# Kernel optimization log

Measured on AMD Instinct MI355X. Metric: run time of the kernel, lower is better.

Reference implementation:

```python
import jax, jax.numpy as jnp
import numpy as np

N_NODES = 50000
N_EDGES = 600000
D = 128
NUM_LAYERS = 2
ALPHA = 0.5
EPS = 1e-12  # torch F.normalize eps


def setup_inputs() -> dict:
    key = jax.random.key(0)
    k1, k2, k3, k4, k5 = jax.random.split(key, 5)
    x = jax.random.normal(k1, (N_NODES, D), dtype=jnp.float32)
    edge_attr = jax.random.normal(k2, (N_EDGES, D), dtype=jnp.float32)
    question_emb = jax.random.normal(k3, (D,), dtype=jnp.float32)
    src = jax.random.randint(k4, (N_EDGES,), 0, N_NODES)
    dst = jax.random.randint(k5, (N_EDGES,), 0, N_NODES)
    edge_index = jnp.stack([src, dst], axis=0).astype(jnp.int64)
    return {"x": x, "edge_attr": edge_attr, "question_emb": question_emb, "edge_index": edge_index}


def reference(x, edge_attr, question_emb, edge_index):
    num_nodes = x.shape[0]
    # edge similarity: cosine of edge_attr rows vs question vector
    ea = edge_attr / jnp.maximum(jnp.linalg.norm(edge_attr, axis=1, keepdims=True), EPS)
    q = question_emb / jnp.maximum(jnp.linalg.norm(question_emb), EPS)
    edge_sim = ea @ q  # [E]
    src, dst = edge_index[0], edge_index[1]
    # degree of destination nodes (constant across layers)
    deg = jax.ops.segment_sum(jnp.ones_like(edge_sim), dst, num_segments=num_nodes)
    deg = jnp.clip(deg, 1.0)[:, None]  # [N,1]
    for _ in range(NUM_LAYERS):
        msgs = x[src] * edge_sim[:, None]                              # [E,D] gather + scale
        x_new = jax.ops.segment_sum(msgs, dst, num_segments=num_nodes)  # [N,D] scatter-add
        x_new = x_new / deg                                             # mean aggregation
        x = ALPHA * x + (1.0 - ALPHA) * x_new                           # residual blend
    return x
```

## Files before the change

### kernel.cpp

```cpp
#include <hip/hip_runtime.h>
#include <hip/hip_fp16.h>
#include <math.h>

#define N_NODES 50000
#define N_EDGES 600000
#define D 128
#define EPS 1e-12f
#define CAP 64

__global__ void cvt_kernel(const float* __restrict__ x, ushort* __restrict__ xh) {
    int i = blockIdx.x * blockDim.x + threadIdx.x;
    if (i >= N_NODES * D / 4) return;
    float4 v = ((const float4*)x)[i];
    ushort4 h;
    h.x = __half_as_ushort(__float2half(v.x));
    h.y = __half_as_ushort(__float2half(v.y));
    h.z = __half_as_ushort(__float2half(v.z));
    h.w = __half_as_ushort(__float2half(v.w));
    ((ushort4*)xh)[i] = h;
}

__global__ void edge_fill_kernel(const float* __restrict__ ea,
                                 const float* __restrict__ q,
                                 const int* __restrict__ src,
                                 const int* __restrict__ dst,
                                 int* __restrict__ cnt,
                                 int2* __restrict__ bucket,
                                 int* __restrict__ ovf_cnt,
                                 int4* __restrict__ ovf) {
    int gid  = blockIdx.x * blockDim.x + threadIdx.x;
    int wave = gid >> 6;
    if (wave >= N_EDGES / 2) return;
    int lane = threadIdx.x & 63;
    int half = lane >> 5;
    int l32  = lane & 31;
    int e    = 2 * wave + half;

    float4 v  = ((const float4*)(ea + (size_t)e * D))[l32];
    float4 qv = ((const float4*)q)[l32];
    float dot = v.x * qv.x + v.y * qv.y + v.z * qv.z + v.w * qv.w;
    float ss  = v.x * v.x + v.y * v.y + v.z * v.z + v.w * v.w;
    float qs  = qv.x * qv.x + qv.y * qv.y + qv.z * qv.z + qv.w * qv.w;
    #pragma unroll
    for (int off = 16; off > 0; off >>= 1) {
        dot += __shfl_xor(dot, off);
        ss  += __shfl_xor(ss, off);
        qs  += __shfl_xor(qs, off);
    }
    if (l32 == 0) {
        float sim = dot / (fmaxf(sqrtf(ss), EPS) * fmaxf(sqrtf(qs), EPS));
        int d    = dst[e];
        int slot = atomicAdd(&cnt[d], 1);
        if (slot < CAP) {
            bucket[(size_t)d * CAP + slot] = make_int2(src[e], __float_as_int(sim));
        } else {
            int oi = atomicAdd(ovf_cnt, 1);
            ovf[oi] = make_int4(d, src[e], __float_as_int(sim), 0);
        }
    }
}

__global__ void agg_kernel(const ushort* __restrict__ xh,
                           const float* __restrict__ xin,
                           const int* __restrict__ cnt,
                           const int2* __restrict__ bucket,
                           float* __restrict__ xout,
                           ushort* __restrict__ xh_out) {
    int gid  = blockIdx.x * blockDim.x + threadIdx.x;
    int node = gid >> 6;
    if (node >= N_NODES) return;
    int lane = threadIdx.x & 63;
    int half = lane >> 5;
    int l32  = lane & 31;

    int n  = cnt[node];
    int nb = (n < CAP) ? n : CAP;

    int sl = 0; float wl = 0.0f;
    if (lane < nb) {
        int2 p = bucket[(size_t)node * CAP + lane];
        sl = p.x; wl = __int_as_float(p.y);
    }

    float4 acc = make_float4(0.0f, 0.0f, 0.0f, 0.0f);
    #pragma unroll 2
    for (int j = half; j < nb; j += 2) {
        int   s = __shfl(sl, j);
        float w = __shfl(wl, j);
        ushort4 hv = ((const ushort4*)(xh + (size_t)s * D))[l32];
        acc.x += __half2float(__ushort_as_half(hv.x)) * w;
        acc.y += __half2float(__ushort_as_half(hv.y)) * w;
        acc.z += __half2float(__ushort_as_half(hv.z)) * w;
        acc.w += __half2float(__ushort_as_half(hv.w)) * w;
    }
    acc.x += __shfl_xor(acc.x, 32);
    acc.y += __shfl_xor(acc.y, 32);
    acc.z += __shfl_xor(acc.z, 32);
    acc.w += __shfl_xor(acc.w, 32);

    if (half == 0) {
        float di = 1.0f / fmaxf((float)n, 1.0f);
        float4 a = ((const float4*)(xin + (size_t)node * D))[l32];
        float4 o;
        o.x = 0.5f * a.x + 0.5f * acc.x * di;
        o.y = 0.5f * a.y + 0.5f * acc.y * di;
        o.z = 0.5f * a.z + 0.5f * acc.z * di;
        o.w = 0.5f * a.w + 0.5f * acc.w * di;
        ((float4*)(xout + (size_t)node * D))[l32] = o;
        if (xh_out) {
            ushort4 h;
            h.x = __half_as_ushort(__float2half(o.x));
            h.y = __half_as_ushort(__float2half(o.y));
            h.z = __half_as_ushort(__float2half(o.z));
            h.w = __half_as_ushort(__float2half(o.w));
            ((ushort4*)(xh_out + (size_t)node * D))[l32] = h;
        }
    }
}

__global__ void ovf_fix_kernel(const float* __restrict__ xin,
                               const int* __restrict__ cnt,
                               const int* __restrict__ ovf_cnt,
                               const int4* __restrict__ ovf,
                               float* __restrict__ xout,
                               ushort* __restrict__ xh_out) {
    int t = threadIdx.x;
    int m = *ovf_cnt;
    for (int i = 0; i < m; ++i) {
        int4 p = ovf[i];
        int d = p.x, s = p.y;
        float w  = __int_as_float(p.z);
        float di = 1.0f / fmaxf((float)cnt[d], 1.0f);
        float r  = xout[(size_t)d * D + t] + 0.5f * w * di * xin[(size_t)s * D + t];
        xout[(size_t)d * D + t] = r;
        if (xh_out) xh_out[(size_t)d * D + t] = __half_as_ushort(__float2half(r));
    }
}

extern "C" void kernel_launch(void* const* d_in, const int* in_sizes, int n_in,
                              void* d_out, int out_size, void* d_ws, size_t ws_size,
                              hipStream_t stream) {
    const float* x  = (const float*)d_in[0];
    const float* ea = (const float*)d_in[1];
    const float* q  = (const float*)d_in[2];
    const int*   ei = (const int*)d_in[3];
    const int* src = ei;
    const int* dst = ei + N_EDGES;
    float* out = (float*)d_out;

    float*  x1      = (float*)d_ws;
    ushort* xh      = (ushort*)(x1 + (size_t)N_NODES * D);
    ushort* x1h     = xh + (size_t)N_NODES * D;
    int2*   bucket  = (int2*)(x1h + (size_t)N_NODES * D);
    int*    cnt     = (int*)(bucket + (size_t)N_NODES * CAP);
    int*    ovf_cnt = cnt + N_NODES;
    int4*   ovf     = (int4*)(cnt + N_NODES + 4);

    hipMemsetAsync(cnt, 0, (size_t)(N_NODES + 4) * sizeof(int), stream);

    cvt_kernel<<<(N_NODES * D / 4 + 255) / 256, 256, 0, stream>>>(x, xh);

    {
        long long threads = (long long)(N_EDGES / 2) * 64;
        int blocks = (int)((threads + 255) / 256);
        edge_fill_kernel<<<blocks, 256, 0, stream>>>(ea, q, src, dst,
                                                     cnt, bucket, ovf_cnt, ovf);
    }

    const int agg_blocks = (int)(((long long)N_NODES * 64 + 255) / 256);
    agg_kernel<<<agg_blocks, 256, 0, stream>>>(xh,  x,  cnt, bucket, x1,  x1h);
    ovf_fix_kernel<<<1, 128, 0, stream>>>(x,  cnt, ovf_cnt, ovf, x1, x1h);
    agg_kernel<<<agg_blocks, 256, 0, stream>>>(x1h, x1, cnt, bucket, out, (ushort*)0);
    ovf_fix_kernel<<<1, 128, 0, stream>>>(x1, cnt, ovf_cnt, ovf, out, (ushort*)0);
}
```

Baseline: 536.6 us.

## Batch 16 independent neighbor row loads per wave in aggregation kernel

The aggregation kernel now has each full 64-lane wave read one half2 (4 bytes) of every neighbor row, instead of splitting the wave into two halves that alternate neighbors and read 8 bytes each. Neighbor offsets are computed up front and 16 gathers are issued back to back before any accumulation, which raises memory-level parallelism and drops the final cross-half reduction. Lanes with no edge default to the node's own row with zero weight, so the first 16 loads are always issued even for low-degree nodes. That adds wasted loads and more registers per thread, which may reduce occupancy.

```diff
diff --git a/kernel.cpp b/kernel.cpp
--- a/kernel.cpp
+++ b/kernel.cpp
@@ -70,51 +70,73 @@
     int node = gid >> 6;
     if (node >= N_NODES) return;
     int lane = threadIdx.x & 63;
-    int half = lane >> 5;
-    int l32  = lane & 31;
 
     int n  = cnt[node];
     int nb = (n < CAP) ? n : CAP;
 
-    int sl = 0; float wl = 0.0f;
+    int sl = node; float wl = 0.0f;
     if (lane < nb) {
         int2 p = bucket[(size_t)node * CAP + lane];
         sl = p.x; wl = __int_as_float(p.y);
     }
 
-    float4 acc = make_float4(0.0f, 0.0f, 0.0f, 0.0f);
-    #pragma unroll 2
-    for (int j = half; j < nb; j += 2) {
+    const uint* base = (const uint*)xh;
+    float accx = 0.0f, accy = 0.0f;
+
+    uint off0[16];
+    #pragma unroll
+    for (int j = 0; j < 16; ++j) {
+        int s = __shfl(sl, j);
+        off0[j] = (uint)s * (D / 2) + lane;
+    }
+    uint u0[16];
+    #pragma unroll
+    for (int j = 0; j < 16; ++j) u0[j] = base[off0[j]];
+    #pragma unroll
+    for (int j = 0; j < 16; ++j) {
+        float w = __shfl(wl, j);
+        __half2 h2 = *reinterpret_cast<__half2*>(&u0[j]);
+        float2 f = __half22float2(h2);
+        accx += f.x * w; accy += f.y * w;
+    }
+
+    if (nb > 16) {
+        uint off1[16];
+        #pragma unroll
+        for (int j = 0; j < 16; ++j) {
+            int s = __shfl(sl, 16 + j);
+            off1[j] = (uint)s * (D / 2) + lane;
+        }
+        uint u1[16];
+        #pragma unroll
+        for (int j = 0; j < 16; ++j) u1[j] = base[off1[j]];
+        #pragma unroll
+        for (int j = 0; j < 16; ++j) {
+            float w = __shfl(wl, 16 + j);
+            __half2 h2 = *reinterpret_cast<__half2*>(&u1[j]);
+            float2 f = __half22float2(h2);
+            accx += f.x * w; accy += f.y * w;
+        }
+    }
+
+    for (int j = 32; j < nb; ++j) {
         int   s = __shfl(sl, j);
         float w = __shfl(wl, j);
-        ushort4 hv = ((const ushort4*)(xh + (size_t)s * D))[l32];
-        acc.x += __half2float(__ushort_as_half(hv.x)) * w;
-        acc.y += __half2float(__ushort_as_half(hv.y)) * w;
-        acc.z += __half2float(__ushort_as_half(hv.z)) * w;
-        acc.w += __half2float(__ushort_as_half(hv.w)) * w;
+        uint u = base[(uint)s * (D / 2) + lane];
+        __half2 h2 = *reinterpret_cast<__half2*>(&u);
+        float2 f = __half22float2(h2);
+        accx += f.x * w; accy += f.y * w;
     }
-    acc.x += __shfl_xor(acc.x, 32);
-    acc.y += __shfl_xor(acc.y, 32);
-    acc.z += __shfl_xor(acc.z, 32);
-    acc.w += __shfl_xor(acc.w, 32);
 
-    if (half == 0) {
-        float di = 1.0f / fmaxf((float)n, 1.0f);
-        float4 a = ((const float4*)(xin + (size_t)node * D))[l32];
-        float4 o;
-        o.x = 0.5f * a.x + 0.5f * acc.x * di;
-        o.y = 0.5f * a.y + 0.5f * acc.y * di;
-        o.z = 0.5f * a.z + 0.5f * acc.z * di;
-        o.w = 0.5f * a.w + 0.5f * acc.w * di;
-        ((float4*)(xout + (size_t)node * D))[l32] = o;
-        if (xh_out) {
-            ushort4 h;
-            h.x = __half_as_ushort(__float2half(o.x));
-            h.y = __half_as_ushort(__float2half(o.y));
-            h.z = __half_as_ushort(__float2half(o.z));
-            h.w = __half_as_ushort(__float2half(o.w));
-            ((ushort4*)(xh_out + (size_t)node * D))[l32] = h;
-        }
+    float di = 1.0f / fmaxf((float)n, 1.0f);
+    float2 a = ((const float2*)xin)[(size_t)node * (D / 2) + lane];
+    float2 o;
+    o.x = 0.5f * a.x + 0.5f * accx * di;
+    o.y = 0.5f * a.y + 0.5f * accy * di;
+    ((float2*)xout)[(size_t)node * (D / 2) + lane] = o;
+    if (xh_out) {
+        __half2 hh = __floats2half2_rn(o.x, o.y);
+        ((uint*)xh_out)[(size_t)node * (D / 2) + lane] = *reinterpret_cast<uint*>(&hh);
     }
 }
 
```

Measured after the change: 521.7 us. 1.03x faster.

## Restructure aggregation into 16-lane groups with batched gathers and fused overflow handling

Applied to the files above, without the earlier changes.

Aggregation now splits each wavefront into four 16-lane groups, each loading a full 256-byte half-precision row with 16-byte loads. Neighbour gathers are issued in batches of four to raise memory-level parallelism, and padding lanes reuse a valid source with zero weight. The separate overflow-fix kernels and the memset are folded into the aggregation and conversion kernels, which removes launches. Edge-attribute reads use nontemporal loads to avoid polluting the cache. Every aggregation thread now scans the overflow list, which costs extra reads if overflow ever occurs.

```diff
diff --git a/kernel.cpp b/kernel.cpp
--- a/kernel.cpp
+++ b/kernel.cpp
@@ -8,16 +8,21 @@
 #define EPS 1e-12f
 #define CAP 64
 
-__global__ void cvt_kernel(const float* __restrict__ x, ushort* __restrict__ xh) {
+typedef float f32x4 __attribute__((ext_vector_type(4)));
+
+__global__ void prep_kernel(const float* __restrict__ x, ushort* __restrict__ xh,
+                            int* __restrict__ cnt) {
     int i = blockIdx.x * blockDim.x + threadIdx.x;
-    if (i >= N_NODES * D / 4) return;
-    float4 v = ((const float4*)x)[i];
-    ushort4 h;
-    h.x = __half_as_ushort(__float2half(v.x));
-    h.y = __half_as_ushort(__float2half(v.y));
-    h.z = __half_as_ushort(__float2half(v.z));
-    h.w = __half_as_ushort(__float2half(v.w));
-    ((ushort4*)xh)[i] = h;
+    if (i < N_NODES + 4) cnt[i] = 0;
+    if (i < N_NODES * D / 4) {
+        float4 v = ((const float4*)x)[i];
+        ushort4 h;
+        h.x = __half_as_ushort(__float2half(v.x));
+        h.y = __half_as_ushort(__float2half(v.y));
+        h.z = __half_as_ushort(__float2half(v.z));
+        h.w = __half_as_ushort(__float2half(v.w));
+        ((ushort4*)xh)[i] = h;
+    }
 }
 
 __global__ void edge_fill_kernel(const float* __restrict__ ea,
@@ -36,7 +41,7 @@
     int l32  = lane & 31;
     int e    = 2 * wave + half;
 
-    float4 v  = ((const float4*)(ea + (size_t)e * D))[l32];
+    f32x4 v  = __builtin_nontemporal_load(((const f32x4*)(ea + (size_t)e * D)) + l32);
     float4 qv = ((const float4*)q)[l32];
     float dot = v.x * qv.x + v.y * qv.y + v.z * qv.z + v.w * qv.w;
     float ss  = v.x * v.x + v.y * v.y + v.z * v.z + v.w * v.w;
@@ -60,80 +65,121 @@
     }
 }
 
+__device__ __forceinline__ void acc8(uint4 v, float w,
+                                     float& a0, float& a1, float& a2, float& a3,
+                                     float& a4, float& a5, float& a6, float& a7) {
+    float2 f;
+    f = __half22float2(*reinterpret_cast<const __half2*>(&v.x)); a0 += f.x * w; a1 += f.y * w;
+    f = __half22float2(*reinterpret_cast<const __half2*>(&v.y)); a2 += f.x * w; a3 += f.y * w;
+    f = __half22float2(*reinterpret_cast<const __half2*>(&v.z)); a4 += f.x * w; a5 += f.y * w;
+    f = __half22float2(*reinterpret_cast<const __half2*>(&v.w)); a6 += f.x * w; a7 += f.y * w;
+}
+
 __global__ void agg_kernel(const ushort* __restrict__ xh,
                            const float* __restrict__ xin,
                            const int* __restrict__ cnt,
                            const int2* __restrict__ bucket,
+                           const int* __restrict__ ovf_cnt,
+                           const int4* __restrict__ ovf,
                            float* __restrict__ xout,
                            ushort* __restrict__ xh_out) {
     int gid  = blockIdx.x * blockDim.x + threadIdx.x;
     int node = gid >> 6;
     if (node >= N_NODES) return;
     int lane = threadIdx.x & 63;
-    int half = lane >> 5;
-    int l32  = lane & 31;
+    int g    = lane >> 4;
+    int l16  = lane & 15;
 
     int n  = cnt[node];
     int nb = (n < CAP) ? n : CAP;
 
-    int sl = 0; float wl = 0.0f;
+    int sl = node; float wl = 0.0f;
     if (lane < nb) {
         int2 p = bucket[(size_t)node * CAP + lane];
         sl = p.x; wl = __int_as_float(p.y);
     }
-
-    float4 acc = make_float4(0.0f, 0.0f, 0.0f, 0.0f);
-    #pragma unroll 2
-    for (int j = half; j < nb; j += 2) {
-        int   s = __shfl(sl, j);
-        float w = __shfl(wl, j);
-        ushort4 hv = ((const ushort4*)(xh + (size_t)s * D))[l32];
-        acc.x += __half2float(__ushort_as_half(hv.x)) * w;
-        acc.y += __half2float(__ushort_as_half(hv.y)) * w;
-        acc.z += __half2float(__ushort_as_half(hv.z)) * w;
-        acc.w += __half2float(__ushort_as_half(hv.w)) * w;
-    }
-    acc.x += __shfl_xor(acc.x, 32);
-    acc.y += __shfl_xor(acc.y, 32);
-    acc.z += __shfl_xor(acc.z, 32);
-    acc.w += __shfl_xor(acc.w, 32);
-
-    if (half == 0) {
+    int s0 = __shfl(sl, 0);
+    if (lane >= nb) sl = s0;
+
+    const uint4* base = (const uint4*)xh;
+    float a0 = 0, a1 = 0, a2 = 0, a3 = 0, a4 = 0, a5 = 0, a6 = 0, a7 = 0;
+
+    {
+        int   e0 = g,      e1 = 4 + g,  e2 = 8 + g,  e3 = 12 + g;
+        int   s_0 = __shfl(sl, e0), s_1 = __shfl(sl, e1), s_2 = __shfl(sl, e2), s_3 = __shfl(sl, e3);
+        float w_0 = __shfl(wl, e0), w_1 = __shfl(wl, e1), w_2 = __shfl(wl, e2), w_3 = __shfl(wl, e3);
+        uint4 v_0 = base[(size_t)s_0 * 16 + l16];
+        uint4 v_1 = base[(size_t)s_1 * 16 + l16];
+        uint4 v_2 = base[(size_t)s_2 * 16 + l16];
+        uint4 v_3 = base[(size_t)s_3 * 16 + l16];
+        acc8(v_0, w_0, a0, a1, a2, a3, a4, a5, a6, a7);
+        acc8(v_1, w_1, a0, a1, a2, a3, a4, a5, a6, a7);
+        acc8(v_2, w_2, a0, a1, a2, a3, a4, a5, a6, a7);
+        acc8(v_3, w_3, a0, a1, a2, a3, a4, a5, a6, a7);
+    }
+    if (nb > 16) {
+        int   e0 = 16 + g, e1 = 20 + g, e2 = 24 + g, e3 = 28 + g;
+        int   s_0 = __shfl(sl, e0), s_1 = __shfl(sl, e1), s_2 = __shfl(sl, e2), s_3 = __shfl(sl, e3);
+        float w_0 = __shfl(wl, e0), w_1 = __shfl(wl, e1), w_2 = __shfl(wl, e2), w_3 = __shfl(wl, e3);
+        uint4 v_0 = base[(size_t)s_0 * 16 + l16];
+        uint4 v_1 = base[(size_t)s_1 * 16 + l16];
+        uint4 v_2 = base[(size_t)s_2 * 16 + l16];
+        uint4 v_3 = base[(size_t)s_3 * 16 + l16];
+        acc8(v_0, w_0, a0, a1, a2, a3, a4, a5, a6, a7);
+        acc8(v_1, w_1, a0, a1, a2, a3, a4, a5, a6, a7);
+        acc8(v_2, w_2, a0, a1, a2, a3, a4, a5, a6, a7);
+        acc8(v_3, w_3, a0, a1, a2, a3, a4, a5, a6, a7);
+    }
+    for (int js = 8; 4 * js < nb; ++js) {
+        int   e0 = 4 * js + g;
+        int   s_0 = __shfl(sl, e0);
+        float w_0 = __shfl(wl, e0);
+        uint4 v_0 = base[(size_t)s_0 * 16 + l16];
+        acc8(v_0, w_0, a0, a1, a2, a3, a4, a5, a6, a7);
+    }
+
+    #define RED(A) A += __shfl_xor(A, 16); A += __shfl_xor(A, 32);
+    RED(a0) RED(a1) RED(a2) RED(a3) RED(a4) RED(a5) RED(a6) RED(a7)
+    #undef RED
+
+    int m = *ovf_cnt;
+    if (m > 0) {
+        for (int i = 0; i < m; ++i) {
+            int4 p = ovf[i];
+            if (p.x == node) {
+                float w = __int_as_float(p.z);
+                const float* r = xin + (size_t)p.y * D + l16 * 8;
+                a0 += w * r[0]; a1 += w * r[1]; a2 += w * r[2]; a3 += w * r[3];
+                a4 += w * r[4]; a5 += w * r[5]; a6 += w * r[6]; a7 += w * r[7];
+            }
+        }
+    }
+
+    if (g < 2) {
         float di = 1.0f / fmaxf((float)n, 1.0f);
-        float4 a = ((const float4*)(xin + (size_t)node * D))[l32];
+        size_t idx = (size_t)node * 32 + l16 * 2 + g;
+        float4 a = ((const float4*)xin)[idx];
         float4 o;
-        o.x = 0.5f * a.x + 0.5f * acc.x * di;
-        o.y = 0.5f * a.y + 0.5f * acc.y * di;
-        o.z = 0.5f * a.z + 0.5f * acc.z * di;
-        o.w = 0.5f * a.w + 0.5f * acc.w * di;
-        ((float4*)(xout + (size_t)node * D))[l32] = o;
+        if (g == 0) {
+            o.x = 0.5f * a.x + 0.5f * a0 * di;
+            o.y = 0.5f * a.y + 0.5f * a1 * di;
+            o.z = 0.5f * a.z + 0.5f * a2 * di;
+            o.w = 0.5f * a.w + 0.5f * a3 * di;
+        } else {
+            o.x = 0.5f * a.x + 0.5f * a4 * di;
+            o.y = 0.5f * a.y + 0.5f * a5 * di;
+            o.z = 0.5f * a.z + 0.5f * a6 * di;
+            o.w = 0.5f * a.w + 0.5f * a7 * di;
+        }
+        ((float4*)xout)[idx] = o;
         if (xh_out) {
-            ushort4 h;
-            h.x = __half_as_ushort(__float2half(o.x));
-            h.y = __half_as_ushort(__float2half(o.y));
-            h.z = __half_as_ushort(__float2half(o.z));
-            h.w = __half_as_ushort(__float2half(o.w));
-            ((ushort4*)(xh_out + (size_t)node * D))[l32] = h;
-        }
-    }
-}
-
-__global__ void ovf_fix_kernel(const float* __restrict__ xin,
-                               const int* __restrict__ cnt,
-                               const int* __restrict__ ovf_cnt,
-                               const int4* __restrict__ ovf,
-                               float* __restrict__ xout,
-                               ushort* __restrict__ xh_out) {
-    int t = threadIdx.x;
-    int m = *ovf_cnt;
-    for (int i = 0; i < m; ++i) {
-        int4 p = ovf[i];
-        int d = p.x, s = p.y;
-        float w  = __int_as_float(p.z);
-        float di = 1.0f / fmaxf((float)cnt[d], 1.0f);
-        float r  = xout[(size_t)d * D + t] + 0.5f * w * di * xin[(size_t)s * D + t];
-        xout[(size_t)d * D + t] = r;
-        if (xh_out) xh_out[(size_t)d * D + t] = __half_as_ushort(__float2half(r));
+            __half2 h0 = __floats2half2_rn(o.x, o.y);
+            __half2 h1 = __floats2half2_rn(o.z, o.w);
+            uint2 u;
+            u.x = *reinterpret_cast<uint*>(&h0);
+            u.y = *reinterpret_cast<uint*>(&h1);
+            ((uint2*)xh_out)[idx] = u;
+        }
     }
 }
 
@@ -156,9 +202,7 @@
     int*    ovf_cnt = cnt + N_NODES;
     int4*   ovf     = (int4*)(cnt + N_NODES + 4);
 
-    hipMemsetAsync(cnt, 0, (size_t)(N_NODES + 4) * sizeof(int), stream);
-
-    cvt_kernel<<<(N_NODES * D / 4 + 255) / 256, 256, 0, stream>>>(x, xh);
+    prep_kernel<<<(N_NODES * D / 4 + 255) / 256, 256, 0, stream>>>(x, xh, cnt);
 
     {
         long long threads = (long long)(N_EDGES / 2) * 64;
@@ -168,8 +212,6 @@
     }
 
     const int agg_blocks = (int)(((long long)N_NODES * 64 + 255) / 256);
-    agg_kernel<<<agg_blocks, 256, 0, stream>>>(xh,  x,  cnt, bucket, x1,  x1h);
-    ovf_fix_kernel<<<1, 128, 0, stream>>>(x,  cnt, ovf_cnt, ovf, x1, x1h);
-    agg_kernel<<<agg_blocks, 256, 0, stream>>>(x1h, x1, cnt, bucket, out, (ushort*)0);
-    ovf_fix_kernel<<<1, 128, 0, stream>>>(x1, cnt, ovf_cnt, ovf, out, (ushort*)0);
-}
+    agg_kernel<<<agg_blocks, 256, 0, stream>>>(xh,  x,  cnt, bucket, ovf_cnt, ovf, x1,  x1h);
+    agg_kernel<<<agg_blocks, 256, 0, stream>>>(x1h, x1, cnt, bucket, ovf_cnt, ovf, out, (ushort*)0);
+}
```

Result: faster. 519.0 us (-3.3%).
